# Performance work log

Hardware: AMD Instinct MI355X
Metric: run time of the kernel (lower is better)

Reference implementation:

```python
import jax, jax.numpy as jnp
import numpy as np
from jax import lax

S = 8  # down/up-sample factor


def _seg_means(x, z):
    """Directional running means between zero-boundaries along the last axis.

    x: float [..., L] values; z: bool [..., L], True at zero-boundary positions.
    For position t strictly between consecutive boundaries (prev, nxt):
      lr[t] = mean(x[prev:t+1]),  rl[t] = mean(x[t:nxt+1]); else keep x[t].
    """
    L = x.shape[-1]
    ar = jnp.arange(L)
    ax = x.ndim - 1
    # last zero index strictly before t (-1 if none)
    idx = jnp.where(z, ar, -1)
    prev = lax.cummax(idx, axis=ax)
    prev = jnp.concatenate(
        [jnp.full(prev.shape[:-1] + (1,), -1, prev.dtype), prev[..., :-1]], axis=-1)
    # first zero index strictly after t (L if none)
    idx2 = jnp.where(z, ar, L)
    nxt = lax.cummin(idx2, axis=ax, reverse=True)
    nxt = jnp.concatenate(
        [nxt[..., 1:], jnp.full(nxt.shape[:-1] + (1,), L, nxt.dtype)], axis=-1)
    valid = (~z) & (prev >= 0) & (nxt < L)
    # padded cumsum: cs0[..., k] = sum(x[..., :k]), length L+1
    cs0 = jnp.concatenate(
        [jnp.zeros(x.shape[:-1] + (1,), x.dtype), jnp.cumsum(x, axis=-1)], axis=-1)
    prev_c = jnp.clip(prev, 0, L - 1)
    nxt_c = jnp.clip(nxt, 0, L - 1)
    sum_lr = cs0[..., 1:] - jnp.take_along_axis(cs0, prev_c, axis=-1)   # x[prev..t]
    sum_rl = jnp.take_along_axis(cs0, nxt_c + 1, axis=-1) - cs0[..., :-1]  # x[t..nxt]
    cnt_lr = jnp.maximum(ar - prev + 1, 1).astype(x.dtype)
    cnt_rl = jnp.maximum(nxt - ar + 1, 1).astype(x.dtype)
    lr = jnp.where(valid, sum_lr / cnt_lr, x)
    rl = jnp.where(valid, sum_rl / cnt_rl, x)
    return lr, rl


def setup_inputs() -> dict:
    key = jax.random.key(0)
    k0, k1 = jax.random.split(key)
    N, C, H, W = 8, 1, 2048, 2048
    x0 = jax.random.normal(k0, (N, C, H, W), dtype=jnp.float32)
    x1 = jax.random.randint(k1, (N, C, H, W), 0, 8, dtype=jnp.int32)
    return {"x0": x0, "x1": x1}


def reference(x0, x1):
    # nearest-neighbor downsample by 8 (matches F.interpolate scale_factor=1/8, mode='nearest')
    x0d = x0[..., ::S, ::S]
    zd = (x1[..., ::S, ::S] == 0)
    # horizontal pass (along rows)
    xh_lr, xh_rl = _seg_means(x0d, zd)
    # vertical pass (along columns) via transpose
    xv_tb, xv_bt = _seg_means(jnp.swapaxes(x0d, -1, -2), jnp.swapaxes(zd, -1, -2))
    y = xh_lr + xh_rl + jnp.swapaxes(xv_tb, -1, -2) + jnp.swapaxes(xv_bt, -1, -2)
    # nearest-neighbor upsample by 8
    y = jnp.repeat(jnp.repeat(y, S, axis=-2), S, axis=-1)
    return y
```

## Files before the change

### kernel.cpp

```cpp
#include <hip/hip_runtime.h>

#define DS   256
#define FULL 2048
#define NIMG 8

__device__ __forceinline__ float seg_fast(float x, bool z, int j,
                                          float* s_cs,
                                          unsigned long long* s_msk,
                                          float* s_ws) {
    const int lane = j & 63;
    const int w    = j >> 6;
    unsigned long long m = __ballot(z);

    float s = x;
    #pragma unroll
    for (int off = 1; off < 64; off <<= 1) {
        float t = __shfl_up(s, off, 64);
        if (lane >= off) s += t;
    }
    if (lane == 63) s_ws[w]  = s;
    if (lane == 0)  s_msk[w] = m;
    __syncthreads();

    float pre = 0.f;
    for (int ww = 0; ww < w; ++ww) pre += s_ws[ww];
    s += pre;
    s_cs[j] = s;

    unsigned long long lo = m & ((1ULL << lane) - 1ULL);
    int prev = -1;
    if (lo) prev = (w << 6) + 63 - __builtin_clzll(lo);
    else {
        for (int ww = w - 1; ww >= 0; --ww) {
            unsigned long long mm = s_msk[ww];
            if (mm) { prev = (ww << 6) + 63 - __builtin_clzll(mm); break; }
        }
    }
    unsigned long long hi = m & ~((2ULL << lane) - 1ULL);
    int nxt = DS;
    if (hi) nxt = (w << 6) + __builtin_ctzll(hi);
    else {
        for (int ww = w + 1; ww < 4; ++ww) {
            unsigned long long mm = s_msk[ww];
            if (mm) { nxt = (ww << 6) + __builtin_ctzll(mm); break; }
        }
    }
    __syncthreads();

    bool valid = (!z) && (prev >= 0) && (nxt < DS);
    if (valid) {
        float cs_j   = s_cs[j];
        float cs_pm1 = (prev > 0) ? s_cs[prev - 1] : 0.f;
        float cs_n   = s_cs[nxt];
        float cs_jm1 = (j > 0) ? s_cs[j - 1] : 0.f;
        return (cs_j - cs_pm1) / (float)(j - prev + 1)
             + (cs_n - cs_jm1) / (float)(nxt - j + 1);
    }
    return 2.f * x;
}

__global__ __launch_bounds__(256) void k_horiz(const float* __restrict__ x0,
                                               const int* __restrict__ x1,
                                               float2* __restrict__ xz,
                                               float* __restrict__ yH) {
    __shared__ float s_cs[DS];
    __shared__ unsigned long long s_msk[4];
    __shared__ float s_ws[4];
    int n = blockIdx.x >> 8;
    int i = blockIdx.x & 255;
    int j = threadIdx.x;
    size_t src = (((size_t)n * FULL) + (size_t)i * 8) * FULL + (size_t)j * 8;
    float x = x0[src];
    bool  z = (x1[src] == 0);
    int d = (n << 16) + (i << 8) + j;
    xz[d] = make_float2(x, z ? 1.f : 0.f);
    yH[d] = seg_fast(x, z, j, s_cs, s_msk, s_ws);
}

__global__ __launch_bounds__(256) void k_vert(const float2* __restrict__ xz,
                                              float* __restrict__ yH) {
    __shared__ float s_cs[DS];
    __shared__ unsigned long long s_msk[4];
    __shared__ float s_ws[4];
    int n = blockIdx.x >> 8;
    int c = blockIdx.x & 255;
    int t = threadIdx.x;
    int d = (n << 16) + (t << 8) + c;
    float2 v = xz[d];
    float r = seg_fast(v.x, v.y != 0.f, t, s_cs, s_msk, s_ws);
    yH[d] += r;
}

__global__ __launch_bounds__(256) void k_up(const float* __restrict__ yD,
                                            float4* __restrict__ out) {
    int gid = blockIdx.x * 256 + threadIdx.x;
    int g2  = gid << 1;
    int j4  = g2 & 511;
    int r   = g2 >> 9;
    int I   = r & 2047;
    int n   = r >> 11;
    int jd  = j4 >> 1;
    float v = yD[(n << 16) + ((I >> 3) << 8) + jd];
    float4 vv = make_float4(v, v, v, v);
    out[g2]     = vv;
    out[g2 + 1] = vv;
}

extern "C" void kernel_launch(void* const* d_in, const int* in_sizes, int n_in,
                              void* d_out, int out_size, void* d_ws, size_t ws_size,
                              hipStream_t stream) {
    const float* x0 = (const float*)d_in[0];
    const int*   x1 = (const int*)d_in[1];
    float* out = (float*)d_out;

    float2* xz = (float2*)d_ws;
    float*  yH = (float*)(xz + NIMG * DS * DS);

    dim3 blk(256);
    k_horiz<<<dim3(NIMG * DS), blk, 0, stream>>>(x0, x1, xz, yH);
    k_vert <<<dim3(NIMG * DS), blk, 0, stream>>>(xz, yH);
    k_up   <<<dim3(16384), blk, 0, stream>>>(yH, (float4*)out);
}
```

Baseline: 51.86 us.

## Merge horizontal and vertical segment passes into one launch; nontemporal upsample stores

The separate horizontal and vertical kernels, which were serialized through an intermediate (x,z) buffer, become a single kernel. Its first half of blocks processes rows and its second half processes columns, each reading the strided input directly. The two results go to separate buffers and are summed in the upsample kernel. The upsample kernel now writes its large output with nontemporal stores. This removes one launch and the dependency between passes. In exchange, column blocks read the original input with a large stride, so those reads are poorly coalesced.

```diff
diff --git a/kernel.cpp b/kernel.cpp
--- a/kernel.cpp
+++ b/kernel.cpp
@@ -3,6 +3,8 @@
 #define DS   256
 #define FULL 2048
 #define NIMG 8
+
+typedef float f32x4 __attribute__((ext_vector_type(4)));
 
 __device__ __forceinline__ float seg_fast(float x, bool z, int j,
                                           float* s_cs,
@@ -59,51 +61,44 @@
     return 2.f * x;
 }
 
-__global__ __launch_bounds__(256) void k_horiz(const float* __restrict__ x0,
-                                               const int* __restrict__ x1,
-                                               float2* __restrict__ xz,
-                                               float* __restrict__ yH) {
+__global__ __launch_bounds__(256) void k_seg(const float* __restrict__ x0,
+                                             const int* __restrict__ x1,
+                                             float* __restrict__ yH,
+                                             float* __restrict__ yV) {
     __shared__ float s_cs[DS];
     __shared__ unsigned long long s_msk[4];
     __shared__ float s_ws[4];
-    int n = blockIdx.x >> 8;
-    int i = blockIdx.x & 255;
-    int j = threadIdx.x;
-    size_t src = (((size_t)n * FULL) + (size_t)i * 8) * FULL + (size_t)j * 8;
+    const int j = threadIdx.x;
+    const bool isCol = blockIdx.x >= (NIMG * DS);
+    const int line = isCol ? (blockIdx.x - NIMG * DS) : blockIdx.x;
+    const int n = line >> 8, ic = line & 255;
+
+    size_t src;
+    if (!isCol) src = ((size_t)(n * FULL + ic * 8)) * FULL + (size_t)j * 8;
+    else        src = ((size_t)(n * FULL + j * 8)) * FULL + (size_t)ic * 8;
     float x = x0[src];
     bool  z = (x1[src] == 0);
-    int d = (n << 16) + (i << 8) + j;
-    xz[d] = make_float2(x, z ? 1.f : 0.f);
-    yH[d] = seg_fast(x, z, j, s_cs, s_msk, s_ws);
+
+    float r = seg_fast(x, z, j, s_cs, s_msk, s_ws);
+
+    if (!isCol) yH[(line << 8) + j] = r;
+    else        yV[(n << 16) + (j << 8) + ic] = r;
 }
 
-__global__ __launch_bounds__(256) void k_vert(const float2* __restrict__ xz,
-                                              float* __restrict__ yH) {
-    __shared__ float s_cs[DS];
-    __shared__ unsigned long long s_msk[4];
-    __shared__ float s_ws[4];
-    int n = blockIdx.x >> 8;
-    int c = blockIdx.x & 255;
-    int t = threadIdx.x;
-    int d = (n << 16) + (t << 8) + c;
-    float2 v = xz[d];
-    float r = seg_fast(v.x, v.y != 0.f, t, s_cs, s_msk, s_ws);
-    yH[d] += r;
-}
-
-__global__ __launch_bounds__(256) void k_up(const float* __restrict__ yD,
-                                            float4* __restrict__ out) {
+__global__ __launch_bounds__(256) void k_up(const float* __restrict__ yH,
+                                            const float* __restrict__ yV,
+                                            f32x4* __restrict__ out) {
     int gid = blockIdx.x * 256 + threadIdx.x;
     int g2  = gid << 1;
     int j4  = g2 & 511;
     int r   = g2 >> 9;
     int I   = r & 2047;
     int n   = r >> 11;
-    int jd  = j4 >> 1;
-    float v = yD[(n << 16) + ((I >> 3) << 8) + jd];
-    float4 vv = make_float4(v, v, v, v);
-    out[g2]     = vv;
-    out[g2 + 1] = vv;
+    int d   = (n << 16) + ((I >> 3) << 8) + (j4 >> 1);
+    float v = yH[d] + yV[d];
+    f32x4 vv = { v, v, v, v };
+    __builtin_nontemporal_store(vv, &out[g2]);
+    __builtin_nontemporal_store(vv, &out[g2 + 1]);
 }
 
 extern "C" void kernel_launch(void* const* d_in, const int* in_sizes, int n_in,
@@ -111,13 +106,12 @@
                               hipStream_t stream) {
     const float* x0 = (const float*)d_in[0];
     const int*   x1 = (const int*)d_in[1];
-    float* out = (float*)d_out;
+    f32x4* out = (f32x4*)d_out;
 
-    float2* xz = (float2*)d_ws;
-    float*  yH = (float*)(xz + NIMG * DS * DS);
+    float* yH = (float*)d_ws;
+    float* yV = yH + NIMG * DS * DS;
 
     dim3 blk(256);
-    k_horiz<<<dim3(NIMG * DS), blk, 0, stream>>>(x0, x1, xz, yH);
-    k_vert <<<dim3(NIMG * DS), blk, 0, stream>>>(xz, yH);
-    k_up   <<<dim3(16384), blk, 0, stream>>>(yH, (float4*)out);
+    k_seg<<<dim3(2 * NIMG * DS), blk, 0, stream>>>(x0, x1, yH, yV);
+    k_up <<<dim3(16384),         blk, 0, stream>>>(yH, yV, out);
 }
```

Result: slower. 84.47 us (+62.9%).
